# Optimization experiments

Measured on AMD Instinct MI355X. Metric: run time of the kernel, lower is better.

## Reference

```python
import jax, jax.numpy as jnp
import numpy as np

BLOCK = 8  # block_size init kwarg


def _process_block(block):
    """Serial Floyd-Steinberg error diffusion within one (BLOCK, BLOCK) tile."""
    def row_step(next_row_err, row):
        row = row + next_row_err  # add errors diffused from the row above
        def px_step(err_right, px):
            old = px + err_right
            new = jnp.where(old > 127.0, 255.0, 0.0)
            e = old - new
            return e * (7.0 / 16.0), (new, e)
        _, (new_row, errs) = jax.lax.scan(px_step, jnp.zeros((), row.dtype), row)
        z = jnp.zeros((1,), errs.dtype)
        # error at x goes to next row at x-1 (3/16), x (5/16), x+1 (1/16)
        nxt = (5.0 / 16.0) * errs \
            + (3.0 / 16.0) * jnp.concatenate([errs[1:], z]) \
            + (1.0 / 16.0) * jnp.concatenate([z, errs[:-1]])
        return nxt, new_row
    _, out = jax.lax.scan(row_step, jnp.zeros((block.shape[1],), block.dtype), block)
    return out


def _halftone(gray):
    """gray: (N, H, W) float32 in [0,255], H and W multiples of BLOCK."""
    N, H, W = gray.shape
    hb, wb = H // BLOCK, W // BLOCK
    blocks = gray.reshape(N, hb, BLOCK, wb, BLOCK).transpose(0, 1, 3, 2, 4)
    blocks = blocks.reshape(N * hb * wb, BLOCK, BLOCK)
    out = jax.vmap(_process_block)(blocks)
    out = out.reshape(N, hb, wb, BLOCK, BLOCK).transpose(0, 1, 3, 2, 4)
    return out.reshape(N, H, W)


def setup_inputs() -> dict:
    key = jax.random.key(0)
    batch = jax.random.uniform(key, (8, 3, 1024, 1024), dtype=jnp.float32)
    return {"batch": batch}


def reference(batch):
    scaled = batch * 255.0  # (B, 3, H, W)
    # cv2.COLOR_BGR2GRAY coefficients on channels [0,1,2] = [B,G,R]
    gray = 0.114 * scaled[:, 0] + 0.587 * scaled[:, 1] + 0.299 * scaled[:, 2]  # (B,H,W)
    # original swapaxes(0,2) -> halftoning runs on a (W, H) layout
    ht = _halftone(gray.transpose(0, 2, 1)).transpose(0, 2, 1)  # (B,H,W), values 0/255
    out = jnp.broadcast_to(ht[:, None, :, :], scaled.shape)
    out = jnp.where(scaled == 0.0, 0.0, out)  # mask: zero input stays zero
    return out / 255.0
```

## Files before the change

### kernel.cpp

```cpp
#include <hip/hip_runtime.h>


#define IMG_H 1024
#define IMG_W 1024
#define NCH   3

typedef float v4f __attribute__((ext_vector_type(4)));

__global__ __launch_bounds__(256, 2)
void fs_halftone_kernel(const float* __restrict__ in, float* __restrict__ out,
                        int n_imgs) {
#pragma clang fp contract(off)
    const int tiles_w = IMG_W / 8;
    const int tiles_per_img = tiles_w * (IMG_H / 8);

    int gtid = blockIdx.x * blockDim.x + threadIdx.x;
    int tile = gtid >> 1;
    int h    = gtid & 1;
    int b  = tile / tiles_per_img;
    if (b >= n_imgs) return;
    int t  = tile % tiles_per_img;
    int th = t / tiles_w;
    int tw = t % tiles_w;

    const size_t imgstride = (size_t)IMG_H * IMG_W;
    const size_t slab_off  = (size_t)(th * 8) * IMG_W + (size_t)(tw * 8) + (size_t)(h * 4);
    const float* base = in  + (size_t)b * NCH * imgstride + slab_off;
    float*      obase = out + (size_t)b * NCH * imgstride + slab_off;

    v4f l0[8], l1[8], l2[8];
#pragma unroll
    for (int r = 0; r < 8; ++r) l0[r] = *(const v4f*)(base + 0 * imgstride + (size_t)r * IMG_W);
#pragma unroll
    for (int r = 0; r < 8; ++r) l1[r] = *(const v4f*)(base + 1 * imgstride + (size_t)r * IMG_W);
#pragma unroll
    for (int r = 0; r < 8; ++r) l2[r] = *(const v4f*)(base + 2 * imgstride + (size_t)r * IMG_W);

    float p[32];
    unsigned int zm0 = 0u, zm1 = 0u, zm2 = 0u;
#pragma unroll
    for (int r = 0; r < 8; ++r) {
#pragma unroll
        for (int k = 0; k < 4; ++k) {
            int idx = r * 4 + k;
            float s0 = l0[r][k] * 255.0f;
            float s1 = l1[r][k] * 255.0f;
            float s2 = l2[r][k] * 255.0f;
            if (s0 == 0.0f) zm0 |= 1u << idx;
            if (s1 == 0.0f) zm1 |= 1u << idx;
            if (s2 == 0.0f) zm2 |= 1u << idx;
            p[idx] = ((0.114f * s0) + (0.587f * s1)) + (0.299f * s2);
        }
    }

    float g[64];
#pragma unroll
    for (int r = 0; r < 8; ++r) {
#pragma unroll
        for (int k = 0; k < 4; ++k) {
            float o = p[r * 4 + k];
            float x = __shfl_xor(o, 1);
            g[r * 8 + k]     = (h == 0) ? o : x;
            g[r * 8 + 4 + k] = (h == 0) ? x : o;
        }
    }

    float nrow[8];
#pragma unroll
    for (int j = 0; j < 8; ++j) nrow[j] = 0.0f;

    unsigned long long hbits = 0ull;

#pragma unroll
    for (int i = 0; i < 8; ++i) {
        float errs[8];
        float er = 0.0f;
#pragma unroll
        for (int j = 0; j < 8; ++j) {
            float px  = g[j * 8 + i] + nrow[j];
            float old = px + er;
            bool  on  = old > 127.0f;
            float nw  = on ? 255.0f : 0.0f;
            float e   = old - nw;
            er = e * 0.4375f;
            errs[j] = e;
            if (on) hbits |= 1ull << (j * 8 + i);
        }
#pragma unroll
        for (int j = 0; j < 8; ++j) {
            float en = (j < 7) ? errs[j + 1] : 0.0f;
            float ep = (j > 0) ? errs[j - 1] : 0.0f;
            nrow[j] = ((0.3125f * errs[j]) + (0.1875f * en)) + (0.0625f * ep);
        }
    }

    int hs = h << 2;
#pragma unroll
    for (int ch = 0; ch < 3; ++ch) {
        unsigned int zm = (ch == 0) ? zm0 : ((ch == 1) ? zm1 : zm2);
#pragma unroll
        for (int r = 0; r < 8; ++r) {
            v4f v;
#pragma unroll
            for (int k = 0; k < 4; ++k) {
                bool on = (hbits >> (r * 8 + hs + k)) & 1ull;
                bool z  = (zm    >> (r * 4 + k)) & 1u;
                v[k] = (on && !z) ? 1.0f : 0.0f;
            }
            *(v4f*)(obase + ch * imgstride + (size_t)r * IMG_W) = v;
        }
    }
}

extern "C" void kernel_launch(void* const* d_in, const int* in_sizes, int n_in,
                              void* d_out, int out_size, void* d_ws, size_t ws_size,
                              hipStream_t stream) {
    const float* in  = (const float*)d_in[0];
    float*       out = (float*)d_out;

    int n_imgs = in_sizes[0] / (NCH * IMG_H * IMG_W);
    int total_threads = 2 * n_imgs * (IMG_H / 8) * (IMG_W / 8);
    int block = 256;
    int grid = (total_threads + block - 1) / block;
    fs_halftone_kernel<<<grid, block, 0, stream>>>(in, out, n_imgs);
}
```

Before: 39.42 us.

## Split each tile across four threads with on-demand column shuffles

Each 8x8 tile is now loaded by four threads that each handle a 2-column slice, instead of two threads with 4-column slices. Per-column gray values are gathered with __shfl inside the serial diffusion loop rather than staging a full 64-entry tile per thread. Channels are loaded and accumulated one at a time to cut live registers, and launch bounds are raised to allow more waves. The aim is higher occupancy and memory parallelism for this bandwidth-bound kernel, at the cost of narrower 8-byte accesses, more shuffles, and redundant serial diffusion in four lanes.

```diff
diff --git a/kernel.cpp b/kernel.cpp
--- a/kernel.cpp
+++ b/kernel.cpp
@@ -5,9 +5,9 @@
 #define IMG_W 1024
 #define NCH   3
 
-typedef float v4f __attribute__((ext_vector_type(4)));
+typedef float v2f __attribute__((ext_vector_type(2)));
 
-__global__ __launch_bounds__(256, 2)
+__global__ __launch_bounds__(256, 6)
 void fs_halftone_kernel(const float* __restrict__ in, float* __restrict__ out,
                         int n_imgs) {
 #pragma clang fp contract(off)
@@ -15,8 +15,9 @@
     const int tiles_per_img = tiles_w * (IMG_H / 8);
 
     int gtid = blockIdx.x * blockDim.x + threadIdx.x;
-    int tile = gtid >> 1;
-    int h    = gtid & 1;
+    int tile = gtid >> 2;
+    int q    = gtid & 3;
+    int lane = threadIdx.x & 63;
     int b  = tile / tiles_per_img;
     if (b >= n_imgs) return;
     int t  = tile % tiles_per_img;
@@ -24,45 +25,54 @@
     int tw = t % tiles_w;
 
     const size_t imgstride = (size_t)IMG_H * IMG_W;
-    const size_t slab_off  = (size_t)(th * 8) * IMG_W + (size_t)(tw * 8) + (size_t)(h * 4);
+    const size_t slab_off  = (size_t)(th * 8) * IMG_W + (size_t)(tw * 8) + (size_t)(q * 2);
     const float* base = in  + (size_t)b * NCH * imgstride + slab_off;
     float*      obase = out + (size_t)b * NCH * imgstride + slab_off;
 
-    v4f l0[8], l1[8], l2[8];
+    float p[16];
+    unsigned int zm0 = 0u, zm1 = 0u, zm2 = 0u;
+
+    {
+        v2f l[8];
 #pragma unroll
-    for (int r = 0; r < 8; ++r) l0[r] = *(const v4f*)(base + 0 * imgstride + (size_t)r * IMG_W);
+        for (int r = 0; r < 8; ++r) l[r] = *(const v2f*)(base + 0 * imgstride + (size_t)r * IMG_W);
 #pragma unroll
-    for (int r = 0; r < 8; ++r) l1[r] = *(const v4f*)(base + 1 * imgstride + (size_t)r * IMG_W);
+        for (int r = 0; r < 8; ++r)
 #pragma unroll
-    for (int r = 0; r < 8; ++r) l2[r] = *(const v4f*)(base + 2 * imgstride + (size_t)r * IMG_W);
-
-    float p[32];
-    unsigned int zm0 = 0u, zm1 = 0u, zm2 = 0u;
+            for (int k = 0; k < 2; ++k) {
+                int idx = r * 2 + k;
+                float s0 = l[r][k] * 255.0f;
+                if (s0 == 0.0f) zm0 |= 1u << idx;
+                p[idx] = 0.114f * s0;
+            }
+    }
+    {
+        v2f l[8];
 #pragma unroll
-    for (int r = 0; r < 8; ++r) {
+        for (int r = 0; r < 8; ++r) l[r] = *(const v2f*)(base + 1 * imgstride + (size_t)r * IMG_W);
 #pragma unroll
-        for (int k = 0; k < 4; ++k) {
-            int idx = r * 4 + k;
-            float s0 = l0[r][k] * 255.0f;
-            float s1 = l1[r][k] * 255.0f;
-            float s2 = l2[r][k] * 255.0f;
-            if (s0 == 0.0f) zm0 |= 1u << idx;
-            if (s1 == 0.0f) zm1 |= 1u << idx;
-            if (s2 == 0.0f) zm2 |= 1u << idx;
-            p[idx] = ((0.114f * s0) + (0.587f * s1)) + (0.299f * s2);
-        }
+        for (int r = 0; r < 8; ++r)
+#pragma unroll
+            for (int k = 0; k < 2; ++k) {
+                int idx = r * 2 + k;
+                float s1 = l[r][k] * 255.0f;
+                if (s1 == 0.0f) zm1 |= 1u << idx;
+                p[idx] = p[idx] + (0.587f * s1);
+            }
     }
-
-    float g[64];
+    {
+        v2f l[8];
 #pragma unroll
-    for (int r = 0; r < 8; ++r) {
+        for (int r = 0; r < 8; ++r) l[r] = *(const v2f*)(base + 2 * imgstride + (size_t)r * IMG_W);
 #pragma unroll
-        for (int k = 0; k < 4; ++k) {
-            float o = p[r * 4 + k];
-            float x = __shfl_xor(o, 1);
-            g[r * 8 + k]     = (h == 0) ? o : x;
-            g[r * 8 + 4 + k] = (h == 0) ? x : o;
-        }
+        for (int r = 0; r < 8; ++r)
+#pragma unroll
+            for (int k = 0; k < 2; ++k) {
+                int idx = r * 2 + k;
+                float s2 = l[r][k] * 255.0f;
+                if (s2 == 0.0f) zm2 |= 1u << idx;
+                p[idx] = p[idx] + (0.299f * s2);
+            }
     }
 
     float nrow[8];
@@ -73,11 +83,17 @@
 
 #pragma unroll
     for (int i = 0; i < 8; ++i) {
+        const int oq = i >> 1, ip = i & 1;
+        float cv[8];
+#pragma unroll
+        for (int j = 0; j < 8; ++j)
+            cv[j] = __shfl(p[j * 2 + ip], (lane & ~3) | oq);
+
         float errs[8];
         float er = 0.0f;
 #pragma unroll
         for (int j = 0; j < 8; ++j) {
-            float px  = g[j * 8 + i] + nrow[j];
+            float px  = cv[j] + nrow[j];
             float old = px + er;
             bool  on  = old > 127.0f;
             float nw  = on ? 255.0f : 0.0f;
@@ -94,20 +110,20 @@
         }
     }
 
-    int hs = h << 2;
+    const int c0 = q * 2;
 #pragma unroll
     for (int ch = 0; ch < 3; ++ch) {
         unsigned int zm = (ch == 0) ? zm0 : ((ch == 1) ? zm1 : zm2);
 #pragma unroll
         for (int r = 0; r < 8; ++r) {
-            v4f v;
+            v2f v;
 #pragma unroll
-            for (int k = 0; k < 4; ++k) {
-                bool on = (hbits >> (r * 8 + hs + k)) & 1ull;
-                bool z  = (zm    >> (r * 4 + k)) & 1u;
+            for (int k = 0; k < 2; ++k) {
+                bool on = (hbits >> (r * 8 + c0 + k)) & 1ull;
+                bool z  = (zm    >> (r * 2 + k)) & 1u;
                 v[k] = (on && !z) ? 1.0f : 0.0f;
             }
-            *(v4f*)(obase + ch * imgstride + (size_t)r * IMG_W) = v;
+            *(v2f*)(obase + ch * imgstride + (size_t)r * IMG_W) = v;
         }
     }
 }
@@ -119,7 +135,7 @@
     float*       out = (float*)d_out;
 
     int n_imgs = in_sizes[0] / (NCH * IMG_H * IMG_W);
-    int total_threads = 2 * n_imgs * (IMG_H / 8) * (IMG_W / 8);
+    int total_threads = 4 * n_imgs * (IMG_H / 8) * (IMG_W / 8);
     int block = 256;
     int grid = (total_threads + block - 1) / block;
     fs_halftone_kernel<<<grid, block, 0, stream>>>(in, out, n_imgs);
```

After: 37.70 us. 4.4% less time.

## Split each 8x8 tile across eight lanes, one column per thread

Applied to the files above, without the earlier changes.

Each tile is now handled by eight threads, one per image column, instead of two threads that each hold four columns. The grayscale values are exchanged with per-step shuffles, and every lane redundantly runs the same serial diffusion and keeps only its own column's output bits. Loads and stores become scalar 4-byte accesses and the occupancy hint rises from 2 to 6. The goal is more threads and lower register pressure for better latency hiding, at the cost of narrower memory accesses, eight times the redundant serial arithmetic and many more shuffles.

```diff
diff --git a/kernel.cpp b/kernel.cpp
--- a/kernel.cpp
+++ b/kernel.cpp
@@ -5,9 +5,7 @@
 #define IMG_W 1024
 #define NCH   3
 
-typedef float v4f __attribute__((ext_vector_type(4)));
-
-__global__ __launch_bounds__(256, 2)
+__global__ __launch_bounds__(256, 6)
 void fs_halftone_kernel(const float* __restrict__ in, float* __restrict__ out,
                         int n_imgs) {
 #pragma clang fp contract(off)
@@ -15,8 +13,9 @@
     const int tiles_per_img = tiles_w * (IMG_H / 8);
 
     int gtid = blockIdx.x * blockDim.x + threadIdx.x;
-    int tile = gtid >> 1;
-    int h    = gtid & 1;
+    int tile = gtid >> 3;
+    int col  = gtid & 7;
+    int lane = threadIdx.x & 63;
     int b  = tile / tiles_per_img;
     if (b >= n_imgs) return;
     int t  = tile % tiles_per_img;
@@ -24,68 +23,59 @@
     int tw = t % tiles_w;
 
     const size_t imgstride = (size_t)IMG_H * IMG_W;
-    const size_t slab_off  = (size_t)(th * 8) * IMG_W + (size_t)(tw * 8) + (size_t)(h * 4);
-    const float* base = in  + (size_t)b * NCH * imgstride + slab_off;
-    float*      obase = out + (size_t)b * NCH * imgstride + slab_off;
+    const size_t col_off   = (size_t)(th * 8) * IMG_W + (size_t)(tw * 8) + (size_t)col;
+    const float* base = in  + (size_t)b * NCH * imgstride + col_off;
+    float*      obase = out + (size_t)b * NCH * imgstride + col_off;
 
-    v4f l0[8], l1[8], l2[8];
+    float a0[8], a1[8], a2[8];
 #pragma unroll
-    for (int r = 0; r < 8; ++r) l0[r] = *(const v4f*)(base + 0 * imgstride + (size_t)r * IMG_W);
+    for (int r = 0; r < 8; ++r) a0[r] = base[0 * imgstride + (size_t)r * IMG_W];
 #pragma unroll
-    for (int r = 0; r < 8; ++r) l1[r] = *(const v4f*)(base + 1 * imgstride + (size_t)r * IMG_W);
+    for (int r = 0; r < 8; ++r) a1[r] = base[1 * imgstride + (size_t)r * IMG_W];
 #pragma unroll
-    for (int r = 0; r < 8; ++r) l2[r] = *(const v4f*)(base + 2 * imgstride + (size_t)r * IMG_W);
+    for (int r = 0; r < 8; ++r) a2[r] = base[2 * imgstride + (size_t)r * IMG_W];
 
-    float p[32];
+    float p[8];
     unsigned int zm0 = 0u, zm1 = 0u, zm2 = 0u;
 #pragma unroll
     for (int r = 0; r < 8; ++r) {
-#pragma unroll
-        for (int k = 0; k < 4; ++k) {
-            int idx = r * 4 + k;
-            float s0 = l0[r][k] * 255.0f;
-            float s1 = l1[r][k] * 255.0f;
-            float s2 = l2[r][k] * 255.0f;
-            if (s0 == 0.0f) zm0 |= 1u << idx;
-            if (s1 == 0.0f) zm1 |= 1u << idx;
-            if (s2 == 0.0f) zm2 |= 1u << idx;
-            p[idx] = ((0.114f * s0) + (0.587f * s1)) + (0.299f * s2);
-        }
-    }
-
-    float g[64];
-#pragma unroll
-    for (int r = 0; r < 8; ++r) {
-#pragma unroll
-        for (int k = 0; k < 4; ++k) {
-            float o = p[r * 4 + k];
-            float x = __shfl_xor(o, 1);
-            g[r * 8 + k]     = (h == 0) ? o : x;
-            g[r * 8 + 4 + k] = (h == 0) ? x : o;
-        }
+        float s0 = a0[r] * 255.0f;
+        float s1 = a1[r] * 255.0f;
+        float s2 = a2[r] * 255.0f;
+        if (s0 == 0.0f) zm0 |= 1u << r;
+        if (s1 == 0.0f) zm1 |= 1u << r;
+        if (s2 == 0.0f) zm2 |= 1u << r;
+        p[r] = ((0.114f * s0) + (0.587f * s1)) + (0.299f * s2);
     }
 
     float nrow[8];
 #pragma unroll
     for (int j = 0; j < 8; ++j) nrow[j] = 0.0f;
 
-    unsigned long long hbits = 0ull;
+    unsigned int ob = 0u;
 
 #pragma unroll
     for (int i = 0; i < 8; ++i) {
+        float cv[8];
+#pragma unroll
+        for (int j = 0; j < 8; ++j)
+            cv[j] = __shfl(p[j], (lane & ~7) | i);
+
         float errs[8];
         float er = 0.0f;
+        unsigned int onb = 0u;
 #pragma unroll
         for (int j = 0; j < 8; ++j) {
-            float px  = g[j * 8 + i] + nrow[j];
+            float px  = cv[j] + nrow[j];
             float old = px + er;
             bool  on  = old > 127.0f;
             float nw  = on ? 255.0f : 0.0f;
             float e   = old - nw;
             er = e * 0.4375f;
             errs[j] = e;
-            if (on) hbits |= 1ull << (j * 8 + i);
+            if (on) onb |= 1u << j;
         }
+        if (col == i) ob = onb;
 #pragma unroll
         for (int j = 0; j < 8; ++j) {
             float en = (j < 7) ? errs[j + 1] : 0.0f;
@@ -94,20 +84,14 @@
         }
     }
 
-    int hs = h << 2;
 #pragma unroll
     for (int ch = 0; ch < 3; ++ch) {
         unsigned int zm = (ch == 0) ? zm0 : ((ch == 1) ? zm1 : zm2);
 #pragma unroll
         for (int r = 0; r < 8; ++r) {
-            v4f v;
-#pragma unroll
-            for (int k = 0; k < 4; ++k) {
-                bool on = (hbits >> (r * 8 + hs + k)) & 1ull;
-                bool z  = (zm    >> (r * 4 + k)) & 1u;
-                v[k] = (on && !z) ? 1.0f : 0.0f;
-            }
-            *(v4f*)(obase + ch * imgstride + (size_t)r * IMG_W) = v;
+            bool on = (ob >> r) & 1u;
+            bool z  = (zm >> r) & 1u;
+            obase[ch * imgstride + (size_t)r * IMG_W] = (on && !z) ? 1.0f : 0.0f;
         }
     }
 }
@@ -119,7 +103,7 @@
     float*       out = (float*)d_out;
 
     int n_imgs = in_sizes[0] / (NCH * IMG_H * IMG_W);
-    int total_threads = 2 * n_imgs * (IMG_H / 8) * (IMG_W / 8);
+    int total_threads = 8 * n_imgs * (IMG_H / 8) * (IMG_W / 8);
     int block = 256;
     int grid = (total_threads + block - 1) / block;
     fs_halftone_kernel<<<grid, block, 0, stream>>>(in, out, n_imgs);
```

Result: faster. 38.40 us (-2.6%).
